# Kernel tuning notes

Hardware: AMD Instinct MI355X
Metric: run time of the kernel (lower is better)

The kernel has to match this reference:

```python
import jax, jax.numpy as jnp
import numpy as np

B, C, H, WD = 256, 512, 28, 28
NCLS = 20


def setup_inputs() -> dict:
    key = jax.random.key(0)
    k1, k2, k3, k4, k5 = jax.random.split(key, 5)
    x = jax.random.normal(k1, (B, C, H, WD), dtype=jnp.float32)
    fmap = jax.random.normal(k2, (B, C, H, WD), dtype=jnp.float32)
    label = jax.random.randint(k3, (B, NCLS), 0, 2, dtype=jnp.int32)  # multi-hot
    W = jax.random.normal(k4, (NCLS, C), dtype=jnp.float32) * 0.02  # fc.weight
    b = jax.random.normal(k5, (NCLS,), dtype=jnp.float32) * 0.02    # fc.bias
    return {"x": x, "fmap": fmap, "label": label, "W": W, "b": b}


def reference(x, fmap, label, W, b):
    # AvgPool2d(28) over the full 28x28 map -> [B, C]
    pooled = jnp.mean(x, axis=(2, 3))
    # Linear(512, 20)
    logits = pooled @ W.T + b  # [B, 20]
    # Per-sample multi-hot gather-sum of classifier weight rows.
    # Original detaches the weight (weight.data round-trip), so stop_gradient.
    Wsg = jax.lax.stop_gradient(W)
    reweight = label.astype(jnp.float32) @ Wsg  # [B, C]
    out_map = fmap * reweight[:, :, None, None]  # [B, C, H, W]
    return (logits, out_map)
```

## Files before the change

### kernel.cpp

```cpp
#include <hip/hip_runtime.h>

#define BATCH 256
#define CH    512
#define HW    784
#define HW4   196
#define NCLS  20

__global__ __launch_bounds__(128) void fused_pool_mul(
    const float* __restrict__ x, const float* __restrict__ fmap,
    const int*   __restrict__ label, const float* __restrict__ W,
    float* __restrict__ pooled, float* __restrict__ out_map)
{
    const int bid = blockIdx.x;
    const int b   = bid >> 9;
    const int c   = bid & 511;
    const int tid = threadIdx.x;

    float rw = 0.0f;
#pragma unroll
    for (int k = 0; k < NCLS; ++k)
        rw += (float)label[b * NCLS + k] * W[k * CH + c];

    const long long base = (long long)bid * HW;
    const float4* x4 = (const float4*)(x    + base);
    const float4* f4 = (const float4*)(fmap + base);
    float4*       o4 = (float4*)(out_map + base);

    float s = 0.0f;
#pragma unroll
    for (int j = tid; j < HW4; j += 128) {
        float4 xv = x4[j];
        s += (xv.x + xv.y) + (xv.z + xv.w);
        float4 fv = f4[j];
        float4 ov;
        ov.x = fv.x * rw; ov.y = fv.y * rw; ov.z = fv.z * rw; ov.w = fv.w * rw;
        o4[j] = ov;
    }

#pragma unroll
    for (int off = 32; off > 0; off >>= 1)
        s += __shfl_down(s, off, 64);
    __shared__ float partial[2];
    if ((tid & 63) == 0) partial[tid >> 6] = s;
    __syncthreads();
    if (tid == 0)
        pooled[bid] = (partial[0] + partial[1]) * (1.0f / (float)HW);
}

__global__ __launch_bounds__(64) void logits_kernel(
    const float* __restrict__ pooled, const float* __restrict__ W,
    const float* __restrict__ bias, float* __restrict__ logits)
{
    const int b    = blockIdx.x;
    const int lane = threadIdx.x;

    float p[8];
#pragma unroll
    for (int i = 0; i < 8; ++i)
        p[i] = pooled[b * CH + lane + i * 64];

    for (int n = 0; n < NCLS; ++n) {
        float s = 0.0f;
#pragma unroll
        for (int i = 0; i < 8; ++i)
            s += p[i] * W[n * CH + lane + i * 64];
#pragma unroll
        for (int off = 32; off > 0; off >>= 1)
            s += __shfl_down(s, off, 64);
        if (lane == 0)
            logits[b * NCLS + n] = s + bias[n];
    }
}

extern "C" void kernel_launch(void* const* d_in, const int* in_sizes, int n_in,
                              void* d_out, int out_size, void* d_ws, size_t ws_size,
                              hipStream_t stream) {
    const float* x     = (const float*)d_in[0];
    const float* fmap  = (const float*)d_in[1];
    const int*   label = (const int*)  d_in[2];
    const float* W     = (const float*)d_in[3];
    const float* bias  = (const float*)d_in[4];

    float* logits  = (float*)d_out;
    float* out_map = (float*)d_out + BATCH * NCLS;
    float* pooled  = (float*)d_ws;

    fused_pool_mul<<<BATCH * CH, 128, 0, stream>>>(x, fmap, label, W, pooled, out_map);
    logits_kernel<<<BATCH, 64, 0, stream>>>(pooled, W, bias, logits);
}
```

Before: 896.6 us.

## Assign one wavefront per row with 16 rows per wave, drop block sync

The fused pool-and-scale kernel now gives each 64-lane wavefront 16 consecutive (b,c) rows. Each row is loaded as three full float4 vectors plus a 4-lane tail, and the row is reduced with a wave shuffle alone, so the shared-memory and __syncthreads step goes away. Labels are packed into a bitmask once per wave and the reweight uses select instead of a multiply. The launch shrinks from 131072 small blocks to 2048 blocks of 256 threads, which cuts block scheduling overhead. In exchange, each wave issues fewer loads at once per row, which may limit memory-level parallelism on this streaming kernel.

```diff
diff --git a/kernel.cpp b/kernel.cpp
--- a/kernel.cpp
+++ b/kernel.cpp
@@ -4,47 +4,76 @@
 #define CH    512
 #define HW    784
 #define HW4   196
+#define NROWS (BATCH * CH)
 #define NCLS  20
+#define RPW   16
 
-__global__ __launch_bounds__(128) void fused_pool_mul(
+__global__ __launch_bounds__(256) void fused_pool_mul(
     const float* __restrict__ x, const float* __restrict__ fmap,
     const int*   __restrict__ label, const float* __restrict__ W,
     float* __restrict__ pooled, float* __restrict__ out_map)
 {
-    const int bid = blockIdx.x;
-    const int b   = bid >> 9;
-    const int c   = bid & 511;
-    const int tid = threadIdx.x;
+    const int lane = threadIdx.x & 63;
+    const int gw   = blockIdx.x * 4 + (threadIdx.x >> 6);
+    const int row0 = gw * RPW;
+    const int b    = row0 >> 9;
 
-    float rw = 0.0f;
+    unsigned mask = 0u;
 #pragma unroll
     for (int k = 0; k < NCLS; ++k)
-        rw += (float)label[b * NCLS + k] * W[k * CH + c];
+        mask |= (unsigned)(label[b * NCLS + k] != 0) << k;
 
-    const long long base = (long long)bid * HW;
-    const float4* x4 = (const float4*)(x    + base);
-    const float4* f4 = (const float4*)(fmap + base);
-    float4*       o4 = (float4*)(out_map + base);
+    for (int r = 0; r < RPW; ++r) {
+        const int row = row0 + r;
+        const int c   = row & 511;
 
-    float s = 0.0f;
+        float rw = 0.0f;
 #pragma unroll
-    for (int j = tid; j < HW4; j += 128) {
-        float4 xv = x4[j];
-        s += (xv.x + xv.y) + (xv.z + xv.w);
-        float4 fv = f4[j];
-        float4 ov;
-        ov.x = fv.x * rw; ov.y = fv.y * rw; ov.z = fv.z * rw; ov.w = fv.w * rw;
-        o4[j] = ov;
-    }
+        for (int k = 0; k < NCLS; ++k) {
+            float w = W[k * CH + c];
+            rw += ((mask >> k) & 1u) ? w : 0.0f;
+        }
+
+        const long long base = (long long)row * HW;
+        const float4* x4 = (const float4*)(x    + base);
+        const float4* f4 = (const float4*)(fmap + base);
+        float4*       o4 = (float4*)(out_map + base);
+
+        float4 xa = x4[lane];
+        float4 xb = x4[lane + 64];
+        float4 xc = x4[lane + 128];
+        float4 fa = f4[lane];
+        float4 fb = f4[lane + 64];
+        float4 fc = f4[lane + 128];
+        float4 xt = make_float4(0.f, 0.f, 0.f, 0.f);
+        float4 ft = make_float4(0.f, 0.f, 0.f, 0.f);
+        if (lane < 4) {
+            xt = x4[192 + lane];
+            ft = f4[192 + lane];
+        }
+
+        float s = ((xa.x + xa.y) + (xa.z + xa.w))
+                + ((xb.x + xb.y) + (xb.z + xb.w))
+                + ((xc.x + xc.y) + (xc.z + xc.w))
+                + ((xt.x + xt.y) + (xt.z + xt.w));
+
+        float4 oa = make_float4(fa.x * rw, fa.y * rw, fa.z * rw, fa.w * rw);
+        float4 ob = make_float4(fb.x * rw, fb.y * rw, fb.z * rw, fb.w * rw);
+        float4 oc = make_float4(fc.x * rw, fc.y * rw, fc.z * rw, fc.w * rw);
+        o4[lane]       = oa;
+        o4[lane + 64]  = ob;
+        o4[lane + 128] = oc;
+        if (lane < 4) {
+            float4 ot = make_float4(ft.x * rw, ft.y * rw, ft.z * rw, ft.w * rw);
+            o4[192 + lane] = ot;
+        }
 
 #pragma unroll
-    for (int off = 32; off > 0; off >>= 1)
-        s += __shfl_down(s, off, 64);
-    __shared__ float partial[2];
-    if ((tid & 63) == 0) partial[tid >> 6] = s;
-    __syncthreads();
-    if (tid == 0)
-        pooled[bid] = (partial[0] + partial[1]) * (1.0f / (float)HW);
+        for (int off = 32; off > 0; off >>= 1)
+            s += __shfl_down(s, off, 64);
+        if (lane == 0)
+            pooled[row] = s * (1.0f / (float)HW);
+    }
 }
 
 __global__ __launch_bounds__(64) void logits_kernel(
@@ -85,6 +114,6 @@
     float* out_map = (float*)d_out + BATCH * NCLS;
     float* pooled  = (float*)d_ws;
 
-    fused_pool_mul<<<BATCH * CH, 128, 0, stream>>>(x, fmap, label, W, pooled, out_map);
+    fused_pool_mul<<<2048, 256, 0, stream>>>(x, fmap, label, W, pooled, out_map);
     logits_kernel<<<BATCH, 64, 0, stream>>>(pooled, W, bias, logits);
 }
```

Result: slower. 920.0 us (+2.6%).
